# Kernel optimization log

Hardware: AMD Instinct MI355X
Metric: run time of the kernel (lower is better)

Reference implementation:

```python
import jax, jax.numpy as jnp
import numpy as np

HEAD_DIM = 64  # from init_kwargs


def setup_inputs() -> dict:
    key = jax.random.key(0)
    k1, k2, k3, k4 = jax.random.split(key, 4)
    N, B, H, T, D = 6, 2, 12, 1024, 768
    return {
        "qk_stack": jax.random.normal(k1, (N, B, H, T, T), dtype=jnp.float32),
        "input_embedding": jax.random.normal(k2, (B, T, D), dtype=jnp.float32),
        "norm_weight": jnp.ones((D,), dtype=jnp.float32),
        "w1": jax.random.normal(k3, (D, N), dtype=jnp.float32) * 0.02,
        "w2": jax.random.normal(k4, (N, N), dtype=jnp.float32) * 0.1,
        "bias": jnp.zeros((N,), dtype=jnp.float32),
    }


def reference(qk_stack, input_embedding, norm_weight, w1, w2, bias):
    # RMSNorm (torch default eps = dtype eps when eps=None)
    eps = jnp.finfo(input_embedding.dtype).eps
    ms = jnp.mean(jnp.square(input_embedding), axis=-1, keepdims=True)
    normed = input_embedding * jax.lax.rsqrt(ms + eps) * norm_weight  # [B,T,D]
    # tiny MLP: A = GELU(normed @ W1) @ W2 + bias  -> [B,T,N]
    a = jax.nn.gelu(normed @ w1, approximate=False) @ w2 + bias
    e = jnp.exp(a)  # [B,T,N]
    scaling = jnp.asarray(1.0 / np.sqrt(HEAD_DIM), dtype=qk_stack.dtype)
    # sum_i scaling * exp(A[:,:,i])[:,None,None,:] * qk_i  (broadcast over heads+queries)
    return scaling * jnp.einsum("nbhqt,btn->bhqt", qk_stack, e)
```

## Files before the change

kernel.cpp:

```cpp
#include <hip/hip_runtime.h>
#include <hip/hip_bf16.h>
#include <math.h>

#define PN 6
#define PB 2
#define PH 12
#define PT 1024
#define PD 768

#define NBLOCKS 3072
#define NTHREADS 256
#define ITERS_PER_B 4

typedef float f4 __attribute__((ext_vector_type(4)));

__global__ __launch_bounds__(64) void compute_e_kernel(
    const float* __restrict__ x,
    const float* __restrict__ nw,
    const float* __restrict__ w1,
    const float* __restrict__ w2,
    const float* __restrict__ bias,
    float* __restrict__ e_out)
{
    const int row  = blockIdx.x;
    const int lane = threadIdx.x;
    const float* xr = x + (size_t)row * PD;

    float xs[12];
    float sumsq = 0.0f;
#pragma unroll
    for (int k = 0; k < 12; ++k) {
        float v = xr[lane + 64 * k];
        xs[k] = v;
        sumsq += v * v;
    }
#pragma unroll
    for (int off = 32; off; off >>= 1) sumsq += __shfl_xor(sumsq, off, 64);

    const float eps = 1.1920928955078125e-07f;
    const float inv = rsqrtf(sumsq * (1.0f / (float)PD) + eps);

    float p[PN] = {0.f, 0.f, 0.f, 0.f, 0.f, 0.f};
#pragma unroll
    for (int k = 0; k < 12; ++k) {
        const int d = lane + 64 * k;
        const float nv = xs[k] * inv * nw[d];
#pragma unroll
        for (int n = 0; n < PN; ++n) p[n] += nv * w1[d * PN + n];
    }
#pragma unroll
    for (int n = 0; n < PN; ++n) {
#pragma unroll
        for (int off = 32; off; off >>= 1) p[n] += __shfl_xor(p[n], off, 64);
    }

    if (lane == 0) {
        float g[PN];
#pragma unroll
        for (int n = 0; n < PN; ++n) {
            const float v = p[n];
            g[n] = 0.5f * v * (1.0f + erff(v * 0.7071067811865476f));
        }
#pragma unroll
        for (int j = 0; j < PN; ++j) {
            float a = bias[j];
#pragma unroll
            for (int n = 0; n < PN; ++n) a += g[n] * w2[n * PN + j];
            e_out[(size_t)j * (PB * PT) + row] = 0.125f * expf(a);
        }
    }
}

__global__ __launch_bounds__(NTHREADS) void combine_kernel(
    const float* __restrict__ qk,
    const float* __restrict__ e,
    float* __restrict__ out)
{
    const uint32_t T4       = PT / 4;
    const uint32_t PLANE4   = (uint32_t)PB * PH * PT * T4;
    const uint32_t BSTRIDE4 = (uint32_t)PH * PT * T4;
    const uint32_t stride   = (uint32_t)NBLOCKS * NTHREADS;

    const f4* q4 = (const f4*)qk;
    const f4* e4 = (const f4*)e;
    f4* o4 = (f4*)out;

    const uint32_t tid = (uint32_t)blockIdx.x * NTHREADS + threadIdx.x;
    const uint32_t t4  = tid & (T4 - 1);

#pragma unroll
    for (uint32_t b = 0; b < PB; ++b) {
        f4 ev[PN];
#pragma unroll
        for (uint32_t n = 0; n < PN; ++n)
            ev[n] = e4[n * (PB * T4) + b * T4 + t4];

        const uint32_t base = b * BSTRIDE4 + tid;

        f4 qv[ITERS_PER_B][PN];
#pragma unroll
        for (uint32_t j = 0; j < ITERS_PER_B; ++j) {
            const uint32_t i4 = base + j * stride;
#pragma unroll
            for (uint32_t n = 0; n < PN; ++n)
                qv[j][n] = __builtin_nontemporal_load(&q4[n * PLANE4 + i4]);
        }

#pragma unroll
        for (uint32_t j = 0; j < ITERS_PER_B; ++j) {
            f4 acc = qv[j][0] * ev[0];
#pragma unroll
            for (uint32_t n = 1; n < PN; ++n) acc += qv[j][n] * ev[n];
            __builtin_nontemporal_store(acc, &o4[base + j * stride]);
        }
    }
}

extern "C" void kernel_launch(void* const* d_in, const int* in_sizes, int n_in,
                              void* d_out, int out_size, void* d_ws, size_t ws_size,
                              hipStream_t stream) {
    const float* qk   = (const float*)d_in[0];
    const float* x    = (const float*)d_in[1];
    const float* nw   = (const float*)d_in[2];
    const float* w1   = (const float*)d_in[3];
    const float* w2   = (const float*)d_in[4];
    const float* bias = (const float*)d_in[5];
    float* out = (float*)d_out;

    float* e_ws = (float*)d_ws;

    compute_e_kernel<<<PB * PT, 64, 0, stream>>>(x, nw, w1, w2, bias, e_ws);
    combine_kernel<<<NBLOCKS, NTHREADS, 0, stream>>>(qk, e_ws, out);
}
```

Measured before the change: 133.8 us.

## Vectorize e computation, pack four rows per block, loop combine with regular loads

The e-computation kernel now handles four rows per 256-thread block and reads the input and norm weight as float4. It also spreads the GELU and output work across six lanes using shuffles. The combine kernel drops the explicit batch of 24 nontemporal loads held in registers and uses a grid-stride loop unrolled by two with ordinary loads over 2048 blocks. The aim is less launch and serialization overhead in the small kernel and more occupancy in the streaming kernel, at the cost of fewer loads in flight per thread and losing the nontemporal hint on the large qk read.

```diff
diff --git a/kernel.cpp b/kernel.cpp
--- a/kernel.cpp
+++ b/kernel.cpp
@@ -8,13 +8,12 @@
 #define PT 1024
 #define PD 768
 
-#define NBLOCKS 3072
+#define NBLOCKS 2048
 #define NTHREADS 256
-#define ITERS_PER_B 4
 
 typedef float f4 __attribute__((ext_vector_type(4)));
 
-__global__ __launch_bounds__(64) void compute_e_kernel(
+__global__ __launch_bounds__(256) void compute_e_kernel(
     const float* __restrict__ x,
     const float* __restrict__ nw,
     const float* __restrict__ w1,
@@ -22,17 +21,19 @@
     const float* __restrict__ bias,
     float* __restrict__ e_out)
 {
-    const int row  = blockIdx.x;
-    const int lane = threadIdx.x;
-    const float* xr = x + (size_t)row * PD;
+    const int wid  = threadIdx.x >> 6;
+    const int lane = threadIdx.x & 63;
+    const int row  = blockIdx.x * 4 + wid;
+    const f4* xr4  = (const f4*)(x + (size_t)row * PD);
+    const f4* nw4  = (const f4*)nw;
 
-    float xs[12];
+    f4 xs[3];
     float sumsq = 0.0f;
 #pragma unroll
-    for (int k = 0; k < 12; ++k) {
-        float v = xr[lane + 64 * k];
+    for (int k = 0; k < 3; ++k) {
+        f4 v = xr4[lane + 64 * k];
         xs[k] = v;
-        sumsq += v * v;
+        sumsq += v.x * v.x + v.y * v.y + v.z * v.z + v.w * v.w;
     }
 #pragma unroll
     for (int off = 32; off; off >>= 1) sumsq += __shfl_xor(sumsq, off, 64);
@@ -42,11 +43,16 @@
 
     float p[PN] = {0.f, 0.f, 0.f, 0.f, 0.f, 0.f};
 #pragma unroll
-    for (int k = 0; k < 12; ++k) {
-        const int d = lane + 64 * k;
-        const float nv = xs[k] * inv * nw[d];
+    for (int k = 0; k < 3; ++k) {
+        const int d0 = 4 * (lane + 64 * k);
+        const f4 nv = xs[k] * inv * nw4[lane + 64 * k];
+        const float nvc[4] = {nv.x, nv.y, nv.z, nv.w};
 #pragma unroll
-        for (int n = 0; n < PN; ++n) p[n] += nv * w1[d * PN + n];
+        for (int c = 0; c < 4; ++c) {
+            const int d = d0 + c;
+#pragma unroll
+            for (int n = 0; n < PN; ++n) p[n] += nvc[c] * w1[d * PN + n];
+        }
     }
 #pragma unroll
     for (int n = 0; n < PN; ++n) {
@@ -54,20 +60,21 @@
         for (int off = 32; off; off >>= 1) p[n] += __shfl_xor(p[n], off, 64);
     }
 
-    if (lane == 0) {
-        float g[PN];
+    float gl = 0.0f;
+    if (lane < PN) {
+        const float v = p[lane];
+        gl = 0.5f * v * (1.0f + erff(v * 0.7071067811865476f));
+    }
+    float g[PN];
 #pragma unroll
-        for (int n = 0; n < PN; ++n) {
-            const float v = p[n];
-            g[n] = 0.5f * v * (1.0f + erff(v * 0.7071067811865476f));
-        }
+    for (int n = 0; n < PN; ++n) g[n] = __shfl(gl, n, 64);
+
+    if (lane < PN) {
+        const int j = lane;
+        float a = bias[j];
 #pragma unroll
-        for (int j = 0; j < PN; ++j) {
-            float a = bias[j];
-#pragma unroll
-            for (int n = 0; n < PN; ++n) a += g[n] * w2[n * PN + j];
-            e_out[(size_t)j * (PB * PT) + row] = 0.125f * expf(a);
-        }
+        for (int n = 0; n < PN; ++n) a += g[n] * w2[n * PN + j];
+        e_out[(size_t)j * (PB * PT) + row] = 0.125f * expf(a);
     }
 }
 
@@ -95,23 +102,16 @@
         for (uint32_t n = 0; n < PN; ++n)
             ev[n] = e4[n * (PB * T4) + b * T4 + t4];
 
-        const uint32_t base = b * BSTRIDE4 + tid;
-
-        f4 qv[ITERS_PER_B][PN];
+        const uint32_t end = (b + 1) * BSTRIDE4;
+#pragma unroll 2
+        for (uint32_t i4 = b * BSTRIDE4 + tid; i4 < end; i4 += stride) {
+            f4 acc = (f4)(0.0f);
 #pragma unroll
-        for (uint32_t j = 0; j < ITERS_PER_B; ++j) {
-            const uint32_t i4 = base + j * stride;
-#pragma unroll
-            for (uint32_t n = 0; n < PN; ++n)
-                qv[j][n] = __builtin_nontemporal_load(&q4[n * PLANE4 + i4]);
-        }
-
-#pragma unroll
-        for (uint32_t j = 0; j < ITERS_PER_B; ++j) {
-            f4 acc = qv[j][0] * ev[0];
-#pragma unroll
-            for (uint32_t n = 1; n < PN; ++n) acc += qv[j][n] * ev[n];
-            __builtin_nontemporal_store(acc, &o4[base + j * stride]);
+            for (uint32_t n = 0; n < PN; ++n) {
+                const f4 qv = q4[n * PLANE4 + i4];
+                acc += qv * ev[n];
+            }
+            __builtin_nontemporal_store(acc, &o4[i4]);
         }
     }
 }
@@ -129,6 +129,6 @@
 
     float* e_ws = (float*)d_ws;
 
-    compute_e_kernel<<<PB * PT, 64, 0, stream>>>(x, nw, w1, w2, bias, e_ws);
+    compute_e_kernel<<<(PB * PT) / 4, 256, 0, stream>>>(x, nw, w1, w2, bias, e_ws);
     combine_kernel<<<NBLOCKS, NTHREADS, 0, stream>>>(qk, e_ws, out);
 }
```

After: 141.5 us. 5.8% more time.
